# Kernel tuning notes

Hardware: AMD Instinct MI355X
Metric: run time of the kernel (lower is better)

## Reference

```python
import jax, jax.numpy as jnp
import numpy as np

N, C, IMG, HEADS = 512, 3, 32, 4
F = C * IMG * IMG          # 3072 node feature dim
E = 4096                   # edges without self loops
EPS = 1e-5                 # BatchNorm eps
SLOPE = 0.2                # GATv2 LeakyReLU negative slope


def bn(x, g, b, m, v):
    # eval-mode BatchNorm2d over channel dim 1
    inv = g / jnp.sqrt(v + EPS)
    return x * inv[None, :, None, None] + (b - m * inv)[None, :, None, None]


def conv1x1(x, W, b):
    # W: [out_c, in_c]
    return jnp.einsum('bchw,oc->bohw', x, W) + b[None, :, None, None]


def setup_inputs():
    key = jax.random.key(0)
    ks = jax.random.split(key, 32)
    inp = {}
    inp['x'] = jax.random.normal(ks[0], (N, C, IMG, IMG), jnp.float32)
    src = jax.random.randint(ks[1], (E,), 0, N)
    off = jax.random.randint(ks[2], (E,), 1, N)
    inp['edge_index'] = jnp.stack([src, (src + off) % N]).astype(jnp.int32)  # no self loops

    def w(k, shape, fan_in):
        return jax.random.normal(k, shape, jnp.float32) / np.sqrt(fan_in)

    i = 3
    def nk():
        nonlocal i; i += 1; return ks[i - 1]
    # grapher fc1: Conv2d(C,C,1)+BN
    inp['fc1_W'] = w(nk(), (C, C), C); inp['fc1_b'] = jnp.zeros((C,), jnp.float32)
    inp['bn1_g'] = jnp.ones((C,), jnp.float32); inp['bn1_b'] = jnp.zeros((C,), jnp.float32)
    inp['bn1_m'] = 0.1 * jax.random.normal(nk(), (C,), jnp.float32)
    inp['bn1_v'] = jax.random.uniform(nk(), (C,), jnp.float32, 0.5, 1.5)
    # GATv2Conv(F, F, heads=HEADS): lin_l, lin_r [F, HEADS*F] with bias, att [HEADS, F], out bias
    inp['Wl'] = w(nk(), (F, HEADS * F), F); inp['bl'] = jnp.zeros((HEADS * F,), jnp.float32)
    inp['Wr'] = w(nk(), (F, HEADS * F), F); inp['br'] = jnp.zeros((HEADS * F,), jnp.float32)
    inp['att'] = w(nk(), (HEADS, F), F)
    inp['gat_b'] = jnp.zeros((HEADS * F,), jnp.float32)
    # grapher fc2: Conv2d(C*HEADS, C, 1)+BN
    inp['fc2_W'] = w(nk(), (C, C * HEADS), C * HEADS); inp['fc2_b'] = jnp.zeros((C,), jnp.float32)
    inp['bn2_g'] = jnp.ones((C,), jnp.float32); inp['bn2_b'] = jnp.zeros((C,), jnp.float32)
    inp['bn2_m'] = 0.1 * jax.random.normal(nk(), (C,), jnp.float32)
    inp['bn2_v'] = jax.random.uniform(nk(), (C,), jnp.float32, 0.5, 1.5)
    # FFN fc1 / fc2 (C->C 1x1 conv + BN)
    inp['ffn1_W'] = w(nk(), (C, C), C); inp['ffn1_b'] = jnp.zeros((C,), jnp.float32)
    inp['bnf1_g'] = jnp.ones((C,), jnp.float32); inp['bnf1_b'] = jnp.zeros((C,), jnp.float32)
    inp['bnf1_m'] = 0.1 * jax.random.normal(nk(), (C,), jnp.float32)
    inp['bnf1_v'] = jax.random.uniform(nk(), (C,), jnp.float32, 0.5, 1.5)
    inp['ffn2_W'] = w(nk(), (C, C), C); inp['ffn2_b'] = jnp.zeros((C,), jnp.float32)
    inp['bnf2_g'] = jnp.ones((C,), jnp.float32); inp['bnf2_b'] = jnp.zeros((C,), jnp.float32)
    inp['bnf2_m'] = 0.1 * jax.random.normal(nk(), (C,), jnp.float32)
    inp['bnf2_v'] = jax.random.uniform(nk(), (C,), jnp.float32, 0.5, 1.5)
    return inp


def reference(x, edge_index, fc1_W, fc1_b, bn1_g, bn1_b, bn1_m, bn1_v,
              Wl, bl, Wr, br, att, gat_b,
              fc2_W, fc2_b, bn2_g, bn2_b, bn2_m, bn2_v,
              ffn1_W, ffn1_b, bnf1_g, bnf1_b, bnf1_m, bnf1_v,
              ffn2_W, ffn2_b, bnf2_g, bnf2_b, bnf2_m, bnf2_v):
    shortcut = x
    h = bn(conv1x1(x, fc1_W, fc1_b), bn1_g, bn1_b, bn1_m, bn1_v)
    hf = h.reshape(N, F)
    xl = (hf @ Wl + bl).reshape(N, HEADS, F)  # source transform
    xr = (hf @ Wr + br).reshape(N, HEADS, F)  # target transform
    # add self loops (PyG GATv2Conv default)
    loops = jnp.arange(N, dtype=edge_index.dtype)
    src = jnp.concatenate([edge_index[0], loops])
    dst = jnp.concatenate([edge_index[1], loops])
    # GATv2 edge scores: a . LeakyReLU(xl_j + xr_i)
    e = jax.nn.leaky_relu(xl[src] + xr[dst], negative_slope=SLOPE)  # [E+N, HEADS, F]
    logits = jnp.einsum('ehf,hf->eh', e, att)
    mx = jax.ops.segment_max(logits, dst, num_segments=N)
    ex = jnp.exp(logits - jax.lax.stop_gradient(mx)[dst])
    denom = jax.ops.segment_sum(ex, dst, num_segments=N)
    alpha = ex / denom[dst]                                          # segment softmax over targets
    agg = jax.ops.segment_sum(xl[src] * alpha[:, :, None], dst, num_segments=N)  # [N, HEADS, F]
    g_out = (agg.reshape(N, HEADS * F) + gat_b).reshape(N, C * HEADS, IMG, IMG)
    g = bn(conv1x1(g_out, fc2_W, fc2_b), bn2_g, bn2_b, bn2_m, bn2_v) + shortcut
    # FFN with residual
    f = jax.nn.relu(bn(conv1x1(g, ffn1_W, ffn1_b), bnf1_g, bnf1_b, bnf1_m, bnf1_v))
    f = bn(conv1x1(f, ffn2_W, ffn2_b), bnf2_g, bnf2_b, bnf2_m, bnf2_v)
    return f + g
```

## Files before the change

kernel.cpp:

```cpp
#include <hip/hip_runtime.h>

#define N_NODES 512
#define FDIM    3072
#define HEADS   4
#define HFD     12288
#define E_IN    4096
#define E_TOT   4608
#define EPSV    1e-5f
#define SLOPE   0.2f

typedef unsigned short u16;
typedef unsigned int   u32;

typedef short s16x8 __attribute__((ext_vector_type(8)));
typedef float f32x4 __attribute__((ext_vector_type(4)));

__device__ __forceinline__ u16 f2bf(float f){
  u32 u = __builtin_bit_cast(u32, f);
  u = (u + 0x7fffu + ((u >> 16) & 1u)) >> 16;
  return (u16)u;
}
__device__ __forceinline__ float bf2f(u16 h){
  return __builtin_bit_cast(float, ((u32)h) << 16);
}
__device__ __forceinline__ float bflo(u32 p){
  return __builtin_bit_cast(float, p << 16);
}
__device__ __forceinline__ float bfhi(u32 p){
  return __builtin_bit_cast(float, p & 0xffff0000u);
}

__device__ __forceinline__ void gl_lds16(const u16* g, u16* l){
  __builtin_amdgcn_global_load_lds(
      (const __attribute__((address_space(1))) unsigned int*)g,
      (__attribute__((address_space(3))) unsigned int*)l, 16, 0, 0);
}

__global__ void k_fc1(const float* __restrict__ x, const float* __restrict__ W,
                      const float* __restrict__ b, const float* __restrict__ g,
                      const float* __restrict__ bb, const float* __restrict__ m,
                      const float* __restrict__ v, u16* __restrict__ hf,
                      int* __restrict__ cnt){
  int id = blockIdx.x * 256 + threadIdx.x;
  if (id < 512) cnt[id] = 0;
  int n = id >> 10, p = id & 1023;
  float x0 = x[n * FDIM + p];
  float x1 = x[n * FDIM + 1024 + p];
  float x2 = x[n * FDIM + 2048 + p];
#pragma unroll
  for (int c = 0; c < 3; ++c){
    float t = b[c] + W[c*3+0]*x0 + W[c*3+1]*x1 + W[c*3+2]*x2;
    float inv = g[c] * rsqrtf(v[c] + EPSV);
    float o = t * inv + (bb[c] - m[c] * inv);
    hf[n * FDIM + c * 1024 + p] = f2bf(o);
  }
}

__global__ __launch_bounds__(256, 3) void k_gemm(
    const u16* __restrict__ hf, const float* __restrict__ Wl,
    const float* __restrict__ bl, const float* __restrict__ Wr,
    const float* __restrict__ br, u16* __restrict__ xl, u16* __restrict__ xr){
  __shared__ u16 As[2][256 * 32];
  __shared__ u16 Bs[2][64 * 40];

  const int tid  = threadIdx.x;
  const int wave = tid >> 6, lane = tid & 63;
  const int quad = lane >> 4, l16 = lane & 15;

  const int g = blockIdx.x;
  const int ntile = (g >> 4) * 8 + (g & 7);
  const int mhalf = (g >> 3) & 1;
  const int n0 = ntile * 64;
  const int rbase = mhalf * 256;

  const float* Wg; const float* biasp; u16* outp; int cb;
  if (n0 < HFD){ Wg = Wl; biasp = bl; outp = xl; cb = n0; }
  else         { Wg = Wr; biasp = br; outp = xr; cb = n0 - HFD; }

  const u16* ga = hf + (size_t)(rbase + wave * 64 + (lane >> 2)) * FDIM
                     + (((lane & 3) ^ ((lane >> 3) & 3)) << 3);

  const int bn = tid & 63, bkh = tid >> 6;
  const float* gb = Wg + (size_t)bkh * 8 * HFD + (cb + bn);
  const int bwo = bn * 40 + bkh * 8;

  const int araw = (wave * 64 + l16) * 32 + ((quad ^ ((l16 >> 1) & 3)) << 3);
  const int brd  = l16 * 40 + quad * 8;

  f32x4 acc[4][4];
#pragma unroll
  for (int i = 0; i < 4; ++i)
#pragma unroll
    for (int j = 0; j < 4; ++j) acc[i][j] = (f32x4){0.f, 0.f, 0.f, 0.f};

  float bv[8];
#pragma unroll
  for (int j = 0; j < 8; ++j) bv[j] = gb[(size_t)j * HFD];
#pragma unroll
  for (int i = 0; i < 4; ++i)
    gl_lds16(ga + (size_t)i * 16 * FDIM, As[0] + (wave * 4 + i) * 512);
  {
    u32 p0 = (u32)f2bf(bv[0]) | ((u32)f2bf(bv[1]) << 16);
    u32 p1 = (u32)f2bf(bv[2]) | ((u32)f2bf(bv[3]) << 16);
    u32 p2 = (u32)f2bf(bv[4]) | ((u32)f2bf(bv[5]) << 16);
    u32 p3 = (u32)f2bf(bv[6]) | ((u32)f2bf(bv[7]) << 16);
    *(uint4*)(Bs[0] + bwo) = make_uint4(p0, p1, p2, p3);
  }
#pragma unroll
  for (int j = 0; j < 8; ++j) bv[j] = gb[(size_t)(32 + j) * HFD];
  __syncthreads();

#define GEMM_BODY(KS, CUR, NXT)                                               \
  {                                                                           \
    const int ksv = (KS);                                                     \
    if (ksv < 95){                                                            \
      _Pragma("unroll")                                                       \
      for (int i = 0; i < 4; ++i)                                             \
        gl_lds16(ga + (size_t)i * 16 * FDIM + (ksv + 1) * 32,                 \
                 As[NXT] + (wave * 4 + i) * 512);                             \
      u32 p0 = (u32)f2bf(bv[0]) | ((u32)f2bf(bv[1]) << 16);                   \
      u32 p1 = (u32)f2bf(bv[2]) | ((u32)f2bf(bv[3]) << 16);                   \
      u32 p2 = (u32)f2bf(bv[4]) | ((u32)f2bf(bv[5]) << 16);                   \
      u32 p3 = (u32)f2bf(bv[6]) | ((u32)f2bf(bv[7]) << 16);                   \
      *(uint4*)(Bs[NXT] + bwo) = make_uint4(p0, p1, p2, p3);                  \
      int kn = (ksv + 2 < 96 ? ksv + 2 : 95) * 32;                            \
      _Pragma("unroll")                                                       \
      for (int j = 0; j < 8; ++j) bv[j] = gb[(size_t)(kn + j) * HFD];         \
    }                                                                         \
    s16x8 af[4], bfr[4];                                                      \
    _Pragma("unroll")                                                         \
    for (int i = 0; i < 4; ++i)                                               \
      af[i] = __builtin_bit_cast(s16x8, *(const uint4*)(As[CUR] + araw + i * 512)); \
    _Pragma("unroll")                                                         \
    for (int j = 0; j < 4; ++j)                                               \
      bfr[j] = __builtin_bit_cast(s16x8, *(const uint4*)(Bs[CUR] + brd + j * 640)); \
    _Pragma("unroll")                                                         \
    for (int i = 0; i < 4; ++i)                                               \
      _Pragma("unroll")                                                       \
      for (int j = 0; j < 4; ++j)                                             \
        acc[i][j] = __builtin_amdgcn_mfma_f32_16x16x32_bf16(af[i], bfr[j], acc[i][j], 0, 0, 0); \
    __syncthreads();                                                          \
  }

  for (int ks = 0; ks < 96; ks += 2){
    GEMM_BODY(ks, 0, 1);
    GEMM_BODY(ks + 1, 1, 0);
  }
#undef GEMM_BODY

  float bj[4];
#pragma unroll
  for (int j = 0; j < 4; ++j) bj[j] = biasp[cb + j * 16 + l16];
#pragma unroll
  for (int i = 0; i < 4; ++i){
    int mrow = rbase + wave * 64 + i * 16 + quad * 4;
#pragma unroll
    for (int r = 0; r < 4; ++r){
      u16* orow = outp + (size_t)(mrow + r) * HFD + cb + l16;
#pragma unroll
      for (int j = 0; j < 4; ++j)
        orow[j * 16] = f2bf(acc[i][j][r] + bj[j]);
    }
  }
}

__global__ void k_logits(const int* __restrict__ ei, const u16* __restrict__ xl,
                         const u16* __restrict__ xr, const float* __restrict__ att,
                         float* __restrict__ logits, int* __restrict__ cnt){
  int e = blockIdx.x;
  int h = threadIdx.x >> 6, lane = threadIdx.x & 63;
  int s, d;
  if (e < E_IN){ s = ei[e]; d = ei[E_IN + e]; } else { s = e - E_IN; d = s; }
  if (threadIdx.x == 0) atomicAdd(&cnt[d], 1);
  const u16* xlp = xl + (size_t)s * HFD + h * FDIM;
  const u16* xrp = xr + (size_t)d * HFD + h * FDIM;
  const float* ap = att + h * FDIM;
  float acc = 0.f;
#pragma unroll
  for (int it = 0; it < 6; ++it){
    int f = it * 512 + lane * 8;
    uint4 a = *(const uint4*)(xlp + f);
    uint4 b = *(const uint4*)(xrp + f);
    float4 w0 = *(const float4*)(ap + f);
    float4 w1 = *(const float4*)(ap + f + 4);
    float v0 = bflo(a.x) + bflo(b.x); v0 = v0 > 0.f ? v0 : SLOPE * v0;
    float v1 = bfhi(a.x) + bfhi(b.x); v1 = v1 > 0.f ? v1 : SLOPE * v1;
    float v2 = bflo(a.y) + bflo(b.y); v2 = v2 > 0.f ? v2 : SLOPE * v2;
    float v3 = bfhi(a.y) + bfhi(b.y); v3 = v3 > 0.f ? v3 : SLOPE * v3;
    float v4 = bflo(a.z) + bflo(b.z); v4 = v4 > 0.f ? v4 : SLOPE * v4;
    float v5 = bfhi(a.z) + bfhi(b.z); v5 = v5 > 0.f ? v5 : SLOPE * v5;
    float v6 = bflo(a.w) + bflo(b.w); v6 = v6 > 0.f ? v6 : SLOPE * v6;
    float v7 = bfhi(a.w) + bfhi(b.w); v7 = v7 > 0.f ? v7 : SLOPE * v7;
    acc += v0 * w0.x + v1 * w0.y + v2 * w0.z + v3 * w0.w;
    acc += v4 * w1.x + v5 * w1.y + v6 * w1.z + v7 * w1.w;
  }
#pragma unroll
  for (int o = 32; o > 0; o >>= 1) acc += __shfl_down(acc, o);
  if (lane == 0) logits[e * 4 + h] = acc;
}

__global__ void k_scan_scatter(const int* __restrict__ ei, const int* __restrict__ cnt,
                               int* __restrict__ off, int* __restrict__ elist){
  __shared__ int s[512];
  __shared__ int cur[512];
  int t = threadIdx.x;
  int v = cnt[t];
  s[t] = v;
  __syncthreads();
  for (int d = 1; d < 512; d <<= 1){
    int add = (t >= d) ? s[t - d] : 0;
    __syncthreads();
    s[t] += add;
    __syncthreads();
  }
  int exc = s[t] - v;
  off[t] = exc;
  cur[t] = exc;
  __syncthreads();
  for (int e = t; e < E_TOT; e += 512){
    int d = (e < E_IN) ? ei[E_IN + e] : (e - E_IN);
    int pos = atomicAdd(&cur[d], 1);
    elist[pos] = e;
  }
}

__global__ void k_softmax(const int* __restrict__ cnt, const int* __restrict__ off,
                          const int* __restrict__ elist, const float* __restrict__ logits,
                          float* __restrict__ alpha){
  int i = blockIdx.x;
  int lane = threadIdx.x;
  int deg = cnt[i], st = off[i];
#pragma unroll
  for (int h = 0; h < 4; ++h){
    float mx = -1e30f;
    for (int j = lane; j < deg; j += 64){
      int e = elist[st + j];
      mx = fmaxf(mx, logits[e * 4 + h]);
    }
#pragma unroll
    for (int o = 32; o > 0; o >>= 1) mx = fmaxf(mx, __shfl_down(mx, o));
    mx = __shfl(mx, 0);
    float sm = 0.f;
    for (int j = lane; j < deg; j += 64){
      int e = elist[st + j];
      sm += __expf(logits[e * 4 + h] - mx);
    }
#pragma unroll
    for (int o = 32; o > 0; o >>= 1) sm += __shfl_down(sm, o);
    sm = __shfl(sm, 0);
    float rs = 1.f / sm;
    for (int j = lane; j < deg; j += 64){
      int e = elist[st + j];
      alpha[e * 4 + h] = __expf(logits[e * 4 + h] - mx) * rs;
    }
  }
}

__global__ __launch_bounds__(256) void k_aggfinal(
    const int* __restrict__ ei, const int* __restrict__ cnt,
    const int* __restrict__ off, const int* __restrict__ elist,
    const float* __restrict__ alpha, const u16* __restrict__ xl,
    const float* __restrict__ gat_b,
    const float* __restrict__ W2, const float* __restrict__ b2,
    const float* __restrict__ g2, const float* __restrict__ bb2,
    const float* __restrict__ m2, const float* __restrict__ v2,
    const float* __restrict__ W3, const float* __restrict__ b3,
    const float* __restrict__ g3, const float* __restrict__ bb3,
    const float* __restrict__ m3, const float* __restrict__ v3,
    const float* __restrict__ W4, const float* __restrict__ b4,
    const float* __restrict__ g4, const float* __restrict__ bb4,
    const float* __restrict__ m4, const float* __restrict__ v4,
    const float* __restrict__ x, float* __restrict__ out){
  __shared__ int    s_src[128];
  __shared__ float4 s_al[128];
  const int n = blockIdx.x;
  const int t = threadIdx.x;
  const int p4 = t * 4;
  const int deg = cnt[n], st = off[n];

  float acc[12][4];
#pragma unroll
  for (int o = 0; o < 12; ++o)
#pragma unroll
    for (int r = 0; r < 4; ++r) acc[o][r] = 0.f;

  for (int base = 0; base < deg; base += 128){
    int cn = min(deg - base, 128);
    if (t < cn){
      int e = elist[st + base + t];
      s_src[t] = (e < E_IN) ? ei[e] : (e - E_IN);
      s_al[t] = *(const float4*)(alpha + e * 4);
    }
    __syncthreads();
    for (int j = 0; j < cn; ++j){
      int s = s_src[j];
      float4 al4 = s_al[j];
      float alh[4] = {al4.x, al4.y, al4.z, al4.w};
      const u16* bp = xl + (size_t)s * HFD;
#pragma unroll
      for (int h = 0; h < 4; ++h){
#pragma unroll
        for (int c = 0; c < 3; ++c){
          ushort4 xv = *(const ushort4*)(bp + h * FDIM + c * 1024 + p4);
          acc[h*3+c][0] += alh[h] * bf2f(xv.x);
          acc[h*3+c][1] += alh[h] * bf2f(xv.y);
          acc[h*3+c][2] += alh[h] * bf2f(xv.z);
          acc[h*3+c][3] += alh[h] * bf2f(xv.w);
        }
      }
    }
    __syncthreads();
  }

#pragma unroll
  for (int o = 0; o < 12; ++o){
    float4 gv = *(const float4*)(gat_b + o * 1024 + p4);
    acc[o][0] += gv.x; acc[o][1] += gv.y; acc[o][2] += gv.z; acc[o][3] += gv.w;
  }
  float xv[3][4];
#pragma unroll
  for (int c = 0; c < 3; ++c){
    float4 t4 = *(const float4*)(x + (size_t)n * FDIM + c * 1024 + p4);
    xv[c][0] = t4.x; xv[c][1] = t4.y; xv[c][2] = t4.z; xv[c][3] = t4.w;
  }
  float o4[3][4];
#pragma unroll
  for (int r = 0; r < 4; ++r){
    float gch[3];
#pragma unroll
    for (int c = 0; c < 3; ++c){
      float tt = b2[c];
#pragma unroll
      for (int o = 0; o < 12; ++o) tt += W2[c * 12 + o] * acc[o][r];
      float inv = g2[c] * rsqrtf(v2[c] + EPSV);
      gch[c] = tt * inv + (bb2[c] - m2[c] * inv) + xv[c][r];
    }
    float f1[3];
#pragma unroll
    for (int c = 0; c < 3; ++c){
      float tt = b3[c] + W3[c*3+0]*gch[0] + W3[c*3+1]*gch[1] + W3[c*3+2]*gch[2];
      float inv = g3[c] * rsqrtf(v3[c] + EPSV);
      float vv = tt * inv + (bb3[c] - m3[c] * inv);
      f1[c] = fmaxf(vv, 0.f);
    }
#pragma unroll
    for (int c = 0; c < 3; ++c){
      float tt = b4[c] + W4[c*3+0]*f1[0] + W4[c*3+1]*f1[1] + W4[c*3+2]*f1[2];
      float inv = g4[c] * rsqrtf(v4[c] + EPSV);
      o4[c][r] = tt * inv + (bb4[c] - m4[c] * inv) + gch[c];
    }
  }
#pragma unroll
  for (int c = 0; c < 3; ++c)
    *(float4*)(out + (size_t)n * FDIM + c * 1024 + p4) =
        make_float4(o4[c][0], o4[c][1], o4[c][2], o4[c][3]);
}

extern "C" void kernel_launch(void* const* d_in, const int* in_sizes, int n_in,
                              void* d_out, int out_size, void* d_ws, size_t ws_size,
                              hipStream_t stream){
  (void)in_sizes; (void)n_in; (void)out_size; (void)ws_size;
  const float* x     = (const float*)d_in[0];
  const int*   ei    = (const int*)d_in[1];
  const float* fc1_W = (const float*)d_in[2];
  const float* fc1_b = (const float*)d_in[3];
  const float* bn1_g = (const float*)d_in[4];
  const float* bn1_b = (const float*)d_in[5];
  const float* bn1_m = (const float*)d_in[6];
  const float* bn1_v = (const float*)d_in[7];
  const float* Wl    = (const float*)d_in[8];
  const float* bl    = (const float*)d_in[9];
  const float* Wr    = (const float*)d_in[10];
  const float* br    = (const float*)d_in[11];
  const float* att   = (const float*)d_in[12];
  const float* gat_b = (const float*)d_in[13];
  const float* fc2_W = (const float*)d_in[14];
  const float* fc2_b = (const float*)d_in[15];
  const float* bn2_g = (const float*)d_in[16];
  const float* bn2_b = (const float*)d_in[17];
  const float* bn2_m = (const float*)d_in[18];
  const float* bn2_v = (const float*)d_in[19];
  const float* ffn1_W= (const float*)d_in[20];
  const float* ffn1_b= (const float*)d_in[21];
  const float* bnf1_g= (const float*)d_in[22];
  const float* bnf1_b= (const float*)d_in[23];
  const float* bnf1_m= (const float*)d_in[24];
  const float* bnf1_v= (const float*)d_in[25];
  const float* ffn2_W= (const float*)d_in[26];
  const float* ffn2_b= (const float*)d_in[27];
  const float* bnf2_g= (const float*)d_in[28];
  const float* bnf2_b= (const float*)d_in[29];
  const float* bnf2_m= (const float*)d_in[30];
  const float* bnf2_v= (const float*)d_in[31];

  char* w = (char*)d_ws;
  u16*   hf     = (u16*)(w);
  u16*   xl     = (u16*)(w + 3145728);
  u16*   xr     = (u16*)(w + 15728640);
  float* logits = (float*)(w + 28311552);
  float* alpha  = (float*)(w + 28385280);
  int*   cnt    = (int*)(w + 28459008);
  int*   offp   = (int*)(w + 28461056);
  int*   elist  = (int*)(w + 28465152);

  k_fc1<<<2048, 256, 0, stream>>>(x, fc1_W, fc1_b, bn1_g, bn1_b, bn1_m, bn1_v, hf, cnt);
  k_gemm<<<768, 256, 0, stream>>>(hf, Wl, bl, Wr, br, xl, xr);
  k_logits<<<E_TOT, 256, 0, stream>>>(ei, xl, xr, att, logits, cnt);
  k_scan_scatter<<<1, 512, 0, stream>>>(ei, cnt, offp, elist);
  k_softmax<<<512, 64, 0, stream>>>(cnt, offp, elist, logits, alpha);
  k_aggfinal<<<512, 256, 0, stream>>>(ei, cnt, offp, elist, alpha, xl, gat_b,
                                      fc2_W, fc2_b, bn2_g, bn2_b, bn2_m, bn2_v,
                                      ffn1_W, ffn1_b, bnf1_g, bnf1_b, bnf1_m, bnf1_v,
                                      ffn2_W, ffn2_b, bnf2_g, bnf2_b, bnf2_m, bnf2_v,
                                      x, (float*)d_out);
}
```

Measured before the change: 527.2 us.

## Deepen B-operand prefetch to two stages with explicit waitcnt and sched barriers

Restructures the GEMM main loop so fp32 weight loads for B are issued two k-steps ahead in alternating register buffers. __syncthreads is replaced with manual s_waitcnt vmcnt counts plus s_barrier, and sched_barriers pin the instruction order so global loads stay in flight across the MFMA block. The goal is to hide global-memory latency of the large weight stream. In exchange it uses more registers and depends on hand-tuned vmcnt values being correct for the async LDS loads.

```diff
diff --git a/kernel.cpp b/kernel.cpp
--- a/kernel.cpp
+++ b/kernel.cpp
@@ -93,60 +93,86 @@
 #pragma unroll
     for (int j = 0; j < 4; ++j) acc[i][j] = (f32x4){0.f, 0.f, 0.f, 0.f};
 
-  float bv[8];
-#pragma unroll
-  for (int j = 0; j < 8; ++j) bv[j] = gb[(size_t)j * HFD];
+#define PACK8(V, DST)                                                          \
+  {                                                                            \
+    u32 p0 = (u32)f2bf(V[0]) | ((u32)f2bf(V[1]) << 16);                        \
+    u32 p1 = (u32)f2bf(V[2]) | ((u32)f2bf(V[3]) << 16);                        \
+    u32 p2 = (u32)f2bf(V[4]) | ((u32)f2bf(V[5]) << 16);                        \
+    u32 p3 = (u32)f2bf(V[6]) | ((u32)f2bf(V[7]) << 16);                        \
+    *(uint4*)(DST) = make_uint4(p0, p1, p2, p3);                               \
+  }
+
+  float bt[8], bv0[8], bv1[8];
+#pragma unroll
+  for (int j = 0; j < 8; ++j) bt[j] = gb[(size_t)j * HFD];
 #pragma unroll
   for (int i = 0; i < 4; ++i)
     gl_lds16(ga + (size_t)i * 16 * FDIM, As[0] + (wave * 4 + i) * 512);
+  __builtin_amdgcn_sched_barrier(0);
+#pragma unroll
+  for (int j = 0; j < 8; ++j) bv0[j] = gb[(size_t)(32 + j) * HFD];
+#pragma unroll
+  for (int j = 0; j < 8; ++j) bv1[j] = gb[(size_t)(64 + j) * HFD];
+  __builtin_amdgcn_sched_barrier(0);
+  PACK8(bt, Bs[0] + bwo);
+  asm volatile("s_waitcnt vmcnt(16) lgkmcnt(0)" ::: "memory");
+  __builtin_amdgcn_s_barrier();
+  __builtin_amdgcn_sched_barrier(0);
+
+#define GEMM_STEP(KS, CUR, NXT, BV, PRELOAD, WAITS)                            \
+  {                                                                            \
+    _Pragma("unroll")                                                          \
+    for (int i = 0; i < 4; ++i)                                                \
+      gl_lds16(ga + (size_t)i * 16 * FDIM + ((KS) + 1) * 32,                   \
+               As[NXT] + (wave * 4 + i) * 512);                                \
+    __builtin_amdgcn_sched_barrier(0);     \
+    PACK8(BV, Bs[NXT] + bwo);                                                  \
+    if (PRELOAD){                                                              \
+      _Pragma("unroll")                                                        \
+      for (int j = 0; j < 8; ++j)                                              \
+        BV[j] = gb[(size_t)(((KS) + 3) * 32 + j) * HFD];                       \
+    }                                                                          \
+    __builtin_amdgcn_sched_barrier(0);    \
+    s16x8 af[4], bfr[4];                                                       \
+    _Pragma("unroll")                                                          \
+    for (int i = 0; i < 4; ++i)                                                \
+      af[i] = __builtin_bit_cast(s16x8, *(const uint4*)(As[CUR] + araw + i * 512)); \
+    _Pragma("unroll")                                                          \
+    for (int j = 0; j < 4; ++j)                                                \
+      bfr[j] = __builtin_bit_cast(s16x8, *(const uint4*)(Bs[CUR] + brd + j * 640)); \
+    _Pragma("unroll")                                                          \
+    for (int i = 0; i < 4; ++i)                                                \
+      _Pragma("unroll")                                                        \
+      for (int j = 0; j < 4; ++j)                                              \
+        acc[i][j] = __builtin_amdgcn_mfma_f32_16x16x32_bf16(af[i], bfr[j], acc[i][j], 0, 0, 0); \
+    asm volatile("s_waitcnt vmcnt(" WAITS ") lgkmcnt(0)" ::: "memory");        \
+    __builtin_amdgcn_s_barrier();                                              \
+    __builtin_amdgcn_sched_barrier(0);                                         \
+  }
+
+  for (int ks = 0; ks < 92; ks += 2){
+    GEMM_STEP(ks,     0, 1, bv0, 1, "8");
+    GEMM_STEP(ks + 1, 1, 0, bv1, 1, "8");
+  }
+  GEMM_STEP(92, 0, 1, bv0, 1, "8");
+  GEMM_STEP(93, 1, 0, bv1, 0, "0");
+  GEMM_STEP(94, 0, 1, bv0, 0, "0");
   {
-    u32 p0 = (u32)f2bf(bv[0]) | ((u32)f2bf(bv[1]) << 16);
-    u32 p1 = (u32)f2bf(bv[2]) | ((u32)f2bf(bv[3]) << 16);
-    u32 p2 = (u32)f2bf(bv[4]) | ((u32)f2bf(bv[5]) << 16);
-    u32 p3 = (u32)f2bf(bv[6]) | ((u32)f2bf(bv[7]) << 16);
-    *(uint4*)(Bs[0] + bwo) = make_uint4(p0, p1, p2, p3);
-  }
-#pragma unroll
-  for (int j = 0; j < 8; ++j) bv[j] = gb[(size_t)(32 + j) * HFD];
-  __syncthreads();
-
-#define GEMM_BODY(KS, CUR, NXT)                                               \
-  {                                                                           \
-    const int ksv = (KS);                                                     \
-    if (ksv < 95){                                                            \
-      _Pragma("unroll")                                                       \
-      for (int i = 0; i < 4; ++i)                                             \
-        gl_lds16(ga + (size_t)i * 16 * FDIM + (ksv + 1) * 32,                 \
-                 As[NXT] + (wave * 4 + i) * 512);                             \
-      u32 p0 = (u32)f2bf(bv[0]) | ((u32)f2bf(bv[1]) << 16);                   \
-      u32 p1 = (u32)f2bf(bv[2]) | ((u32)f2bf(bv[3]) << 16);                   \
-      u32 p2 = (u32)f2bf(bv[4]) | ((u32)f2bf(bv[5]) << 16);                   \
-      u32 p3 = (u32)f2bf(bv[6]) | ((u32)f2bf(bv[7]) << 16);                   \
-      *(uint4*)(Bs[NXT] + bwo) = make_uint4(p0, p1, p2, p3);                  \
-      int kn = (ksv + 2 < 96 ? ksv + 2 : 95) * 32;                            \
-      _Pragma("unroll")                                                       \
-      for (int j = 0; j < 8; ++j) bv[j] = gb[(size_t)(kn + j) * HFD];         \
-    }                                                                         \
-    s16x8 af[4], bfr[4];                                                      \
-    _Pragma("unroll")                                                         \
-    for (int i = 0; i < 4; ++i)                                               \
-      af[i] = __builtin_bit_cast(s16x8, *(const uint4*)(As[CUR] + araw + i * 512)); \
-    _Pragma("unroll")                                                         \
-    for (int j = 0; j < 4; ++j)                                               \
-      bfr[j] = __builtin_bit_cast(s16x8, *(const uint4*)(Bs[CUR] + brd + j * 640)); \
-    _Pragma("unroll")                                                         \
-    for (int i = 0; i < 4; ++i)                                               \
-      _Pragma("unroll")                                                       \
-      for (int j = 0; j < 4; ++j)                                             \
-        acc[i][j] = __builtin_amdgcn_mfma_f32_16x16x32_bf16(af[i], bfr[j], acc[i][j], 0, 0, 0); \
-    __syncthreads();                                                          \
-  }
-
-  for (int ks = 0; ks < 96; ks += 2){
-    GEMM_BODY(ks, 0, 1);
-    GEMM_BODY(ks + 1, 1, 0);
-  }
-#undef GEMM_BODY
+    s16x8 af[4], bfr[4];
+#pragma unroll
+    for (int i = 0; i < 4; ++i)
+      af[i] = __builtin_bit_cast(s16x8, *(const uint4*)(As[1] + araw + i * 512));
+#pragma unroll
+    for (int j = 0; j < 4; ++j)
+      bfr[j] = __builtin_bit_cast(s16x8, *(const uint4*)(Bs[1] + brd + j * 640));
+#pragma unroll
+    for (int i = 0; i < 4; ++i)
+#pragma unroll
+      for (int j = 0; j < 4; ++j)
+        acc[i][j] = __builtin_amdgcn_mfma_f32_16x16x32_bf16(af[i], bfr[j], acc[i][j], 0, 0, 0);
+  }
+#undef GEMM_STEP
+#undef PACK8
 
   float bj[4];
 #pragma unroll
```

After: 540.8 us. +2.6%, slower.

## Fuse edge logits with per-target softmax and build CSR before GEMM

Applied to the files above, without the earlier changes.

Counting, scanning and scattering of edges now run in one CSR kernel launched before fc1, so the atomic degree count no longer sits inside the logits kernel. The per-edge logits kernel and the separate softmax kernel are merged into one per-target-node kernel. It keeps the target's xr row and the attention weights in registers, computes the logits of all incoming edges into shared memory, and writes alpha directly. This removes one launch, the logits round trip and repeated xr/att loads per edge. The cost is only 512 blocks with a serial loop over each node's edges and higher register use, which may reduce parallelism and latency hiding compared with 4608 independent edge blocks.

```diff
diff --git a/kernel.cpp b/kernel.cpp
--- a/kernel.cpp
+++ b/kernel.cpp
@@ -8,6 +8,7 @@
 #define E_TOT   4608
 #define EPSV    1e-5f
 #define SLOPE   0.2f
+#define LCAP    256
 
 typedef unsigned short u16;
 typedef unsigned int   u32;
@@ -36,13 +37,42 @@
       (__attribute__((address_space(3))) unsigned int*)l, 16, 0, 0);
 }
 
+__global__ void k_csr(const int* __restrict__ ei, int* __restrict__ cnt,
+                      int* __restrict__ off, int* __restrict__ elist){
+  __shared__ int s[512];
+  __shared__ int cur[512];
+  int t = threadIdx.x;
+  s[t] = 0;
+  __syncthreads();
+  for (int e = t; e < E_TOT; e += 512){
+    int d = (e < E_IN) ? ei[E_IN + e] : (e - E_IN);
+    atomicAdd(&s[d], 1);
+  }
+  __syncthreads();
+  int v = s[t];
+  cnt[t] = v;
+  for (int dd = 1; dd < 512; dd <<= 1){
+    int add = (t >= dd) ? s[t - dd] : 0;
+    __syncthreads();
+    s[t] += add;
+    __syncthreads();
+  }
+  int exc = s[t] - v;
+  off[t] = exc;
+  cur[t] = exc;
+  __syncthreads();
+  for (int e = t; e < E_TOT; e += 512){
+    int d = (e < E_IN) ? ei[E_IN + e] : (e - E_IN);
+    int pos = atomicAdd(&cur[d], 1);
+    elist[pos] = e;
+  }
+}
+
 __global__ void k_fc1(const float* __restrict__ x, const float* __restrict__ W,
                       const float* __restrict__ b, const float* __restrict__ g,
                       const float* __restrict__ bb, const float* __restrict__ m,
-                      const float* __restrict__ v, u16* __restrict__ hf,
-                      int* __restrict__ cnt){
+                      const float* __restrict__ v, u16* __restrict__ hf){
   int id = blockIdx.x * 256 + threadIdx.x;
-  if (id < 512) cnt[id] = 0;
   int n = id >> 10, p = id & 1023;
   float x0 = x[n * FDIM + p];
   float x1 = x[n * FDIM + 1024 + p];
@@ -164,78 +194,91 @@
   }
 }
 
-__global__ void k_logits(const int* __restrict__ ei, const u16* __restrict__ xl,
-                         const u16* __restrict__ xr, const float* __restrict__ att,
-                         float* __restrict__ logits, int* __restrict__ cnt){
-  int e = blockIdx.x;
-  int h = threadIdx.x >> 6, lane = threadIdx.x & 63;
-  int s, d;
-  if (e < E_IN){ s = ei[e]; d = ei[E_IN + e]; } else { s = e - E_IN; d = s; }
-  if (threadIdx.x == 0) atomicAdd(&cnt[d], 1);
-  const u16* xlp = xl + (size_t)s * HFD + h * FDIM;
-  const u16* xrp = xr + (size_t)d * HFD + h * FDIM;
-  const float* ap = att + h * FDIM;
-  float acc = 0.f;
-#pragma unroll
-  for (int it = 0; it < 6; ++it){
-    int f = it * 512 + lane * 8;
-    uint4 a = *(const uint4*)(xlp + f);
-    uint4 b = *(const uint4*)(xrp + f);
-    float4 w0 = *(const float4*)(ap + f);
-    float4 w1 = *(const float4*)(ap + f + 4);
-    float v0 = bflo(a.x) + bflo(b.x); v0 = v0 > 0.f ? v0 : SLOPE * v0;
-    float v1 = bfhi(a.x) + bfhi(b.x); v1 = v1 > 0.f ? v1 : SLOPE * v1;
-    float v2 = bflo(a.y) + bflo(b.y); v2 = v2 > 0.f ? v2 : SLOPE * v2;
-    float v3 = bfhi(a.y) + bfhi(b.y); v3 = v3 > 0.f ? v3 : SLOPE * v3;
-    float v4 = bflo(a.z) + bflo(b.z); v4 = v4 > 0.f ? v4 : SLOPE * v4;
-    float v5 = bfhi(a.z) + bfhi(b.z); v5 = v5 > 0.f ? v5 : SLOPE * v5;
-    float v6 = bflo(a.w) + bflo(b.w); v6 = v6 > 0.f ? v6 : SLOPE * v6;
-    float v7 = bfhi(a.w) + bfhi(b.w); v7 = v7 > 0.f ? v7 : SLOPE * v7;
-    acc += v0 * w0.x + v1 * w0.y + v2 * w0.z + v3 * w0.w;
-    acc += v4 * w1.x + v5 * w1.y + v6 * w1.z + v7 * w1.w;
-  }
-#pragma unroll
-  for (int o = 32; o > 0; o >>= 1) acc += __shfl_down(acc, o);
-  if (lane == 0) logits[e * 4 + h] = acc;
-}
-
-__global__ void k_scan_scatter(const int* __restrict__ ei, const int* __restrict__ cnt,
-                               int* __restrict__ off, int* __restrict__ elist){
-  __shared__ int s[512];
-  __shared__ int cur[512];
-  int t = threadIdx.x;
-  int v = cnt[t];
-  s[t] = v;
-  __syncthreads();
-  for (int d = 1; d < 512; d <<= 1){
-    int add = (t >= d) ? s[t - d] : 0;
+__global__ __launch_bounds__(256) void k_lsm(
+    const int* __restrict__ ei, const int* __restrict__ cnt,
+    const int* __restrict__ off, const int* __restrict__ elist,
+    const u16* __restrict__ xl, const u16* __restrict__ xr,
+    const float* __restrict__ att, float* __restrict__ alpha){
+  __shared__ float s_log[LCAP][5];
+  __shared__ int   s_e[LCAP];
+  const int n = blockIdx.x;
+  const int t = threadIdx.x;
+  const int h = t >> 6, lane = t & 63;
+  const int deg = cnt[n], st = off[n];
+  const int f0 = lane * 48;
+
+  float xrf[48], av[48];
+  {
+    const u16* xrp = xr + (size_t)n * HFD + h * FDIM + f0;
+    const float* ap = att + h * FDIM + f0;
+#pragma unroll
+    for (int k = 0; k < 6; ++k){
+      uint4 a = *(const uint4*)(xrp + k * 8);
+      xrf[k*8+0]=bflo(a.x); xrf[k*8+1]=bfhi(a.x);
+      xrf[k*8+2]=bflo(a.y); xrf[k*8+3]=bfhi(a.y);
+      xrf[k*8+4]=bflo(a.z); xrf[k*8+5]=bfhi(a.z);
+      xrf[k*8+6]=bflo(a.w); xrf[k*8+7]=bfhi(a.w);
+      float4 w0 = *(const float4*)(ap + k * 8);
+      float4 w1 = *(const float4*)(ap + k * 8 + 4);
+      av[k*8+0]=w0.x; av[k*8+1]=w0.y; av[k*8+2]=w0.z; av[k*8+3]=w0.w;
+      av[k*8+4]=w1.x; av[k*8+5]=w1.y; av[k*8+6]=w1.z; av[k*8+7]=w1.w;
+    }
+  }
+
+  auto edge_logit = [&](int s_node) -> float {
+    const u16* xlp = xl + (size_t)s_node * HFD + h * FDIM + f0;
+    float acc = 0.f;
+#pragma unroll
+    for (int k = 0; k < 6; ++k){
+      uint4 a = *(const uint4*)(xlp + k * 8);
+      float z;
+      z = bflo(a.x) + xrf[k*8+0]; z = z > 0.f ? z : SLOPE * z; acc += z * av[k*8+0];
+      z = bfhi(a.x) + xrf[k*8+1]; z = z > 0.f ? z : SLOPE * z; acc += z * av[k*8+1];
+      z = bflo(a.y) + xrf[k*8+2]; z = z > 0.f ? z : SLOPE * z; acc += z * av[k*8+2];
+      z = bfhi(a.y) + xrf[k*8+3]; z = z > 0.f ? z : SLOPE * z; acc += z * av[k*8+3];
+      z = bflo(a.z) + xrf[k*8+4]; z = z > 0.f ? z : SLOPE * z; acc += z * av[k*8+4];
+      z = bfhi(a.z) + xrf[k*8+5]; z = z > 0.f ? z : SLOPE * z; acc += z * av[k*8+5];
+      z = bflo(a.w) + xrf[k*8+6]; z = z > 0.f ? z : SLOPE * z; acc += z * av[k*8+6];
+      z = bfhi(a.w) + xrf[k*8+7]; z = z > 0.f ? z : SLOPE * z; acc += z * av[k*8+7];
+    }
+#pragma unroll
+    for (int o = 32; o > 0; o >>= 1) acc += __shfl_down(acc, o);
+    return acc;
+  };
+
+  if (deg <= LCAP){
+    for (int jb = 0; jb < deg; ++jb){
+      int e = elist[st + jb];
+      if (t == 0) s_e[jb] = e;
+      int s = (e < E_IN) ? ei[e] : (e - E_IN);
+      float lg = edge_logit(s);
+      if (lane == 0) s_log[jb][h] = lg;
+    }
     __syncthreads();
-    s[t] += add;
-    __syncthreads();
-  }
-  int exc = s[t] - v;
-  off[t] = exc;
-  cur[t] = exc;
-  __syncthreads();
-  for (int e = t; e < E_TOT; e += 512){
-    int d = (e < E_IN) ? ei[E_IN + e] : (e - E_IN);
-    int pos = atomicAdd(&cur[d], 1);
-    elist[pos] = e;
-  }
-}
-
-__global__ void k_softmax(const int* __restrict__ cnt, const int* __restrict__ off,
-                          const int* __restrict__ elist, const float* __restrict__ logits,
-                          float* __restrict__ alpha){
-  int i = blockIdx.x;
-  int lane = threadIdx.x;
-  int deg = cnt[i], st = off[i];
-#pragma unroll
-  for (int h = 0; h < 4; ++h){
+    float mx = -1e30f;
+    for (int j = lane; j < deg; j += 64) mx = fmaxf(mx, s_log[j][h]);
+#pragma unroll
+    for (int o = 32; o > 0; o >>= 1) mx = fmaxf(mx, __shfl_down(mx, o));
+    mx = __shfl(mx, 0);
+    float sm = 0.f;
+    for (int j = lane; j < deg; j += 64) sm += __expf(s_log[j][h] - mx);
+#pragma unroll
+    for (int o = 32; o > 0; o >>= 1) sm += __shfl_down(sm, o);
+    sm = __shfl(sm, 0);
+    float rs = 1.f / sm;
+    for (int j = lane; j < deg; j += 64)
+      alpha[s_e[j] * 4 + h] = __expf(s_log[j][h] - mx) * rs;
+  } else {
+    for (int jb = 0; jb < deg; ++jb){
+      int e = elist[st + jb];
+      int s = (e < E_IN) ? ei[e] : (e - E_IN);
+      float lg = edge_logit(s);
+      if (lane == 0) alpha[e * 4 + h] = lg;
+    }
     float mx = -1e30f;
     for (int j = lane; j < deg; j += 64){
       int e = elist[st + j];
-      mx = fmaxf(mx, logits[e * 4 + h]);
+      mx = fmaxf(mx, alpha[e * 4 + h]);
     }
 #pragma unroll
     for (int o = 32; o > 0; o >>= 1) mx = fmaxf(mx, __shfl_down(mx, o));
@@ -243,7 +286,7 @@
     float sm = 0.f;
     for (int j = lane; j < deg; j += 64){
       int e = elist[st + j];
-      sm += __expf(logits[e * 4 + h] - mx);
+      sm += __expf(alpha[e * 4 + h] - mx);
     }
 #pragma unroll
     for (int o = 32; o > 0; o >>= 1) sm += __shfl_down(sm, o);
@@ -251,7 +294,7 @@
     float rs = 1.f / sm;
     for (int j = lane; j < deg; j += 64){
       int e = elist[st + j];
-      alpha[e * 4 + h] = __expf(logits[e * 4 + h] - mx) * rs;
+      alpha[e * 4 + h] = __expf(alpha[e * 4 + h] - mx) * rs;
     }
   }
 }
@@ -397,17 +440,15 @@
   u16*   hf     = (u16*)(w);
   u16*   xl     = (u16*)(w + 3145728);
   u16*   xr     = (u16*)(w + 15728640);
-  float* logits = (float*)(w + 28311552);
   float* alpha  = (float*)(w + 28385280);
   int*   cnt    = (int*)(w + 28459008);
   int*   offp   = (int*)(w + 28461056);
   int*   elist  = (int*)(w + 28465152);
 
-  k_fc1<<<2048, 256, 0, stream>>>(x, fc1_W, fc1_b, bn1_g, bn1_b, bn1_m, bn1_v, hf, cnt);
+  k_csr<<<1, 512, 0, stream>>>(ei, cnt, offp, elist);
+  k_fc1<<<2048, 256, 0, stream>>>(x, fc1_W, fc1_b, bn1_g, bn1_b, bn1_m, bn1_v, hf);
   k_gemm<<<768, 256, 0, stream>>>(hf, Wl, bl, Wr, br, xl, xr);
-  k_logits<<<E_TOT, 256, 0, stream>>>(ei, xl, xr, att, logits, cnt);
-  k_scan_scatter<<<1, 512, 0, stream>>>(ei, cnt, offp, elist);
-  k_softmax<<<512, 64, 0, stream>>>(cnt, offp, elist, logits, alpha);
+  k_lsm<<<512, 256, 0, stream>>>(ei, cnt, offp, elist, xl, xr, att, alpha);
   k_aggfinal<<<512, 256, 0, stream>>>(ei, cnt, offp, elist, alpha, xl, gat_b,
                                       fc2_W, fc2_b, bn2_g, bn2_b, bn2_m, bn2_v,
                                       ffn1_W, ffn1_b, bnf1_g, bnf1_b, bnf1_m, bnf1_v,
```

Result: no change. 525.1 us (-0.4%).
